# Optimization experiments

Hardware: AMD Instinct MI355X
Metric: run time of the kernel (lower is better)

The kernel has to match this reference:

```python
import jax, jax.numpy as jnp
import numpy as np

# Static trigram-LM trie configuration (uniform branching K per node).
V_ = 32000; N_ = 3; K_ = 32; S_ = 32; SOS_ = 0; B_ = 32; L_ = 8
U_ = V_ + 1
N_BI = V_ * K_                    # number of bigram nodes
O_ = U_ + N_BI + 1                # offsets/logbs length (bigram block + sentinel)
N_TRI = N_BI * K_                 # number of trigram leaves
G_ = N_TRI
P_ = O_ + G_                      # logps length


def _build_trie():
    """Valid CSR-style flattened trie: children of node at position q live at
    [offsets[q]+q, offsets[q+1]+q+1); every node has exactly K children with
    sorted token ids 0..K-1. ids[p-U_] is the token id of node at position p."""
    rng = np.random.default_rng(0)
    offsets = np.empty(O_, np.int64)
    # unigram v's children occupy positions [U_+v*K_, U_+(v+1)*K_)
    offsets[:U_] = U_ + np.arange(U_) * (K_ - 1)
    # bigram j (position U_+j) children occupy [O_+j*K_, O_+(j+1)*K_)
    offsets[U_:] = (O_ - U_) + np.arange(N_BI + 1) * (K_ - 1)
    ids = np.empty(P_ - U_, np.int32)
    ids[:N_BI] = np.arange(N_BI) % K_       # bigram node token ids
    ids[N_BI] = 0                           # sentinel slot at position O_-1
    ids[N_BI + 1:] = np.arange(N_TRI) % K_  # trigram leaf token ids
    logps = (-rng.uniform(0.1, 10.0, P_)).astype(np.float32)
    logbs = (-rng.uniform(0.01, 2.0, O_)).astype(np.float32)
    return offsets.astype(np.int32), ids, logps, logbs


def setup_inputs() -> dict:
    key = jax.random.key(0)
    k1, k2 = jax.random.split(key)
    offsets, ids, logps, logbs = _build_trie()
    # tokens in [0, 2K): half of them miss in the trie -> exercises backoff path
    hist = jax.random.randint(k1, (L_, B_), 0, 2 * K_, dtype=jnp.int32)
    hidx = jax.random.randint(k2, (B_,), 0, L_, dtype=jnp.int32)
    return {"hist": hist, "hidx": hidx, "offsets": jnp.asarray(offsets),
            "ids": jnp.asarray(ids), "logps": jnp.asarray(logps),
            "logbs": jnp.asarray(logbs), "sos": SOS_, "V": V_, "N": N_,
            "G": G_, "S": S_}


def reference(hist, hidx, offsets, ids, logps, logbs, sos, V, N, G, S):
    B = hist.shape[1]
    M = B * V
    O = offsets.shape[0]
    P = logps.shape[0]
    shift = 0 if 0 <= sos < V else 1
    U = V + shift + 1 % N
    if N == 1:
        return jnp.broadcast_to(logps[:V], (B, V))
    # Always left-pad N-1 sos tokens (equivalent to torch's rem padding; the
    # subsequent window gather makes extra padding harmless).
    pad = N - 1
    hist = jnp.concatenate([jnp.full((pad, B), sos, hist.dtype), hist])
    hidx = hidx + pad
    # context = the N-1 tokens at positions hidx-(N-1) .. hidx-1, per batch
    pos = hidx[None, :] - (N - 1) + jnp.arange(N - 1)[:, None]   # (N-1, B)
    ctx = jnp.take_along_axis(hist, pos, axis=0)                  # (N-1, B)
    if shift:
        ctx = jnp.where(ctx == sos, V, ctx)
    ctx = ctx.astype(ids.dtype)
    srange = jnp.arange(S)
    # first M entries: candidate words v per batch; last B: context pointer
    desc = jnp.concatenate([jnp.tile(jnp.arange(V, dtype=jnp.int32), B),
                            ctx[-1].astype(jnp.int32)])
    last_logps = jnp.tile(logps[:V], B)                           # (M,)
    last_backoffs = jnp.repeat(logbs[desc[M:]], V)                # (M,)
    found = jnp.ones(M + B, bool)
    for n in range(1, N):
        hist_n = jnp.concatenate([jnp.repeat(ctx[-n], V), ctx[-min(n + 1, N - 1)]])
        desc_starts = offsets[desc] + desc
        desc_ends = offsets[desc + 1] + desc + 1
        pos_desc = desc_starts[:, None] + srange[None, :]         # (M+B, S)
        ext = desc_ends[:, None] > pos_desc
        ids_ = ids[jnp.minimum(pos_desc, P - 1) - U]
        ext = ext & (hist_n[:, None] == ids_)
        found = ext.any(1) & found
        desc = jnp.where(found, jnp.where(ext, pos_desc, 0).sum(1), desc)
        logps_desc = logps[desc[:M]]
        if n == N - 1:
            cur_backoffs = jnp.zeros_like(last_backoffs)
        else:
            cur_backoffs = jnp.repeat(
                jnp.where(found[M:], logbs[jnp.minimum(desc[M:], O - 1)], 0.0), V)
        clobber = jnp.isfinite(logps_desc) & found[:M]
        cur_logps = jnp.where(clobber, logps_desc,
                              last_logps + cur_backoffs + last_backoffs)
        last_backoffs = jnp.where(clobber, cur_backoffs, 0.0)
        last_logps = jnp.where(jnp.repeat(hidx >= n, V), cur_logps, last_logps)
    return last_logps.reshape(B, V)
```

## Files before the change

### kernel.cpp

```cpp
#include <hip/hip_runtime.h>
#include <math.h>


#define MAXN 8
#define TPB  1024
#define NW   16
#define BGW  2
#define BGB  32
#define WI   37
#define WO   41

struct PerB {
  int   ctx[MAXN];
  float bo[MAXN];
  float b1;
  int   hp;
};

__device__ __forceinline__ bool find_child(const int* __restrict__ offsets,
                                           const int* __restrict__ ids,
                                           int q, int t, int U, int P, int S,
                                           int* pos_out) {
  int start = offsets[q] + q;
  int end   = offsets[q + 1] + q + 1;
  int n = end - start;
  if (n > S) n = S;
  if (n <= 0) return false;
  int j = (t < n - 1) ? t : (n - 1);
  if (j < 0) j = 0;
  int x = ids[min(start + j, P - 1) - U];
  if (x == t) { *pos_out = start + j; return true; }
  if (x < t) return false;
  int lo = 0, hi = j - 1;
  while (lo < hi) {
    int mid = (lo + hi) >> 1;
    int xm = ids[min(start + mid, P - 1) - U];
    if (xm < t) lo = mid + 1; else hi = mid;
  }
  if (lo < j) {
    int xm = ids[min(start + lo, P - 1) - U];
    if (xm == t) { *pos_out = start + lo; return true; }
  }
  return false;
}

__device__ __forceinline__ float score_v(const int* __restrict__ offsets,
                                         const int* __restrict__ ids,
                                         const float* __restrict__ logps,
                                         const PerB* __restrict__ pbb,
                                         int v, float lp0,
                                         int N, int U, int O, int P, int S) {
  float last_lp = lp0;
  float last_bo = pbb->b1;
  int hp = pbb->hp;
  int desc = v;
  bool found = true;
  float cur_lp = lp0;
  for (int n = 1; n <= N - 1; ++n) {
    int t = pbb->ctx[(N - 1) - n];
    if (found) {
      int pos;
      found = find_child(offsets, ids, desc, t, U, P, S, &pos);
      if (found) { desc = pos; cur_lp = logps[desc]; }
    }
    float cur_bo = (n == N - 1) ? 0.0f : pbb->bo[n];
    bool clobber = isfinite(cur_lp) && found;
    float newlp = clobber ? cur_lp : (last_lp + cur_bo + last_bo);
    last_bo = clobber ? cur_bo : 0.0f;
    if (hp >= n) last_lp = newlp;
  }
  return last_lp;
}

__global__ void __launch_bounds__(TPB, 8)
lm_fused(const int* __restrict__ hist, const int* __restrict__ hidx,
         const int* __restrict__ offsets, const int* __restrict__ ids,
         const float* __restrict__ logps, const float* __restrict__ logbs,
         const int* __restrict__ sos_p, const int* __restrict__ N_p,
         const int* __restrict__ S_p,
         float* __restrict__ out,
         int V, int B, int L, int O, int P) {
  __shared__ PerB s_pb[BGB];
  __shared__ int  ids_w[64 * WI];
  __shared__ int  off_w[64 * WO];
  __shared__ int  s_start1[64], s_n1[64], s_shi[64], s_sho[64];

  const int tid  = threadIdx.x;
  const int lane = tid & 63;
  const int w    = tid >> 6;
  const int vbase = blockIdx.x * 64;
  const int v     = vbase + lane;
  const int b0    = blockIdx.y * BGB;
  const int N = *N_p, S = *S_p, sos = *sos_p;
  const int Nc = (N > 0) ? N : 1;
  const int shift = (0 <= sos && sos < V) ? 0 : 1;
  const int U = V + shift + 1 % Nc;
  const int idsN = P - U;

  const bool fast = (N == 3) && (S == 32);

  if (tid < BGB && N > 1) {
    int b = b0 + tid;
    if (b < B) {
      int pad = N - 1;
      int hp = hidx[b] + pad;
      PerB o;
      o.hp = hp;
      for (int k = 0; k < N - 1; ++k) {
        int r = hp - (N - 1) + k;
        int tok = (r < pad) ? sos : hist[(r - pad) * B + b];
        if (shift && tok == sos) tok = V;
        o.ctx[k] = tok;
      }
      o.b1 = logbs[o.ctx[N - 2]];
      int desc = o.ctx[N - 2];
      bool found = true;
      for (int n = 1; n <= N - 2; ++n) {
        int t = o.ctx[(N - 1) - min(n + 1, N - 1)];
        if (found) {
          int pos;
          found = find_child(offsets, ids, desc, t, U, P, S, &pos);
          if (found) desc = pos;
        }
        o.bo[n] = found ? logbs[min(desc, O - 1)] : 0.0f;
      }
      s_pb[tid] = o;
    }
  }

  if (!fast) {
    __syncthreads();
    if (v < V) {
      float lp0 = logps[v];
      if (N <= 1) {
        for (int ib = w; ib < BGB; ib += NW) {
          int b = b0 + ib;
          if (b < B) out[(size_t)b * V + v] = lp0;
        }
      } else {
        for (int ib = w; ib < BGB; ib += NW) {
          int b = b0 + ib;
          if (b < B)
            out[(size_t)b * V + v] = score_v(offsets, ids, logps, s_pb + ib, v,
                                             lp0, N, U, O, P, S);
        }
      }
    }
    return;
  }

  {
    int row  = tid >> 4;
    int part = tid & 15;
    int vv = vbase + row;
    if (vv < V) {
      int ov  = offsets[vv];
      int ov1 = offsets[vv + 1];
      int start1 = ov + vv;
      int n1 = ov1 + 1 - ov;
      if (n1 > 32) n1 = 32;
      int* myids = ids_w + row * WI;
      int* myoff = off_w + row * WO;
      int aidx0 = start1 - U;
      int sh_i = 0, sh_o = 0;
      bool vec_ok = (start1 >= 0) && (aidx0 >= 0) &&
                    (((aidx0 & ~3) + 36) <= idsN) &&
                    (((start1 & ~3) + 40) <= O);
      if (vec_ok) {
        int ab = aidx0 & ~3;
        sh_i = aidx0 - ab;
        const int4* ip = (const int4*)(ids + ab);
        for (int k = part; k < 9; k += 16) {
          int4 t = ip[k];
          myids[4 * k + 0] = t.x; myids[4 * k + 1] = t.y;
          myids[4 * k + 2] = t.z; myids[4 * k + 3] = t.w;
        }
        int ob = start1 & ~3;
        sh_o = start1 - ob;
        const int4* op = (const int4*)(offsets + ob);
        for (int k = part; k < 10; k += 16) {
          int4 t = op[k];
          myoff[4 * k + 0] = t.x; myoff[4 * k + 1] = t.y;
          myoff[4 * k + 2] = t.z; myoff[4 * k + 3] = t.w;
        }
      } else {
        for (int j = part; j < 36; j += 16) {
          int ii = min(start1 + j, P - 1) - U;
          ii = max(0, min(ii, idsN - 1));
          myids[j] = ids[ii];
        }
        for (int j = part; j < 40; j += 16) {
          int oo = max(0, min(start1 + j, O - 1));
          myoff[j] = offsets[oo];
        }
      }
      if (part == 0) {
        s_start1[row] = start1; s_n1[row] = n1;
        s_shi[row] = sh_i;      s_sho[row] = sh_o;
      }
    } else if (part == 0) {
      s_start1[row] = 0; s_n1[row] = 0; s_shi[row] = 0; s_sho[row] = 0;
    }
  }
  __syncthreads();
  if (v >= V) return;

  float lp0 = logps[v];
  const int start1 = s_start1[lane];
  const int n1     = s_n1[lane];
  const int sh_i   = s_shi[lane];
  const int sh_o   = s_sho[lane];
  const int* myids = ids_w + lane * WI;
  const int* myoff = off_w + lane * WO;

  const int nb = min(BGB, B - b0);

  int j1v[BGW];
  int cc1[BGW];
  int cc2[BGW];
  unsigned f1m = 0, l2m = 0;
#pragma unroll
  for (int i = 0; i < BGW; ++i) {
    int ib = w * BGW + i;
    if (ib >= nb) { j1v[i] = 0; cc1[i] = v; cc2[i] = v; continue; }
    int t1 = s_pb[ib].ctx[1];
    bool found = false;
    int j1 = 0;
    if (n1 > 0) {
      int jj = (t1 < n1 - 1) ? t1 : (n1 - 1);
      if (jj < 0) jj = 0;
      int x = myids[sh_i + jj];
      if (x == t1) { found = true; j1 = jj; }
      else if (x > t1) {
        int lo = 0, hi = jj - 1;
        while (lo < hi) {
          int mid = (lo + hi) >> 1;
          if (myids[sh_i + mid] < t1) lo = mid + 1; else hi = mid;
        }
        if (lo < jj && myids[sh_i + lo] == t1) { found = true; j1 = lo; }
      }
    }
    int c1 = start1 + j1;
    j1v[i] = j1;
    int a1 = min(c1, P - 1);
    cc1[i] = a1;
    int t0 = s_pb[ib].ctx[0];
    int o1 = myoff[sh_o + j1];
    int o2 = myoff[sh_o + j1 + 1];
    int start2 = o1 + c1;
    int n2 = o2 + 1 - o1;
    if (n2 > 32) n2 = 32;
    bool l2ok = found && (n2 > 0);
    int jj2 = (t0 < n2 - 1) ? t0 : (n2 - 1);
    if (jj2 < 0) jj2 = 0;
    int c2 = min(start2 + jj2, P - 1);
    cc2[i] = l2ok ? c2 : a1;
    f1m |= (found ? 1u : 0u) << i;
    l2m |= (l2ok ? 1u : 0u) << i;
  }

  float lp1v[BGW];
  int   x2v[BGW];
#pragma unroll
  for (int i = 0; i < BGW; ++i) lp1v[i] = logps[cc1[i]];
#pragma unroll
  for (int i = 0; i < BGW; ++i) {
    int ii = cc2[i] - U;
    ii = max(0, min(ii, idsN - 1));
    x2v[i] = __builtin_nontemporal_load(ids + ii);
  }

  float sp2v[BGW];
#pragma unroll
  for (int i = 0; i < BGW; ++i) {
    int ib = w * BGW + i;
    sp2v[i] = 0.0f;
    if (ib < nb) {
      bool l2ok = (l2m >> i) & 1u;
      if (l2ok && x2v[i] == s_pb[ib].ctx[0])
        sp2v[i] = __builtin_nontemporal_load(logps + cc2[i]);
    }
  }

#pragma unroll
  for (int i = 0; i < BGW; ++i) {
    int ib = w * BGW + i;
    if (ib >= nb) continue;
    bool found = (f1m >> i) & 1u;
    bool l2ok  = (l2m >> i) & 1u;
    int   hp = s_pb[ib].hp;
    float bo1 = s_pb[ib].bo[1];
    float last_bo = s_pb[ib].b1;
    float last_lp = lp0;

    float lp1 = found ? lp1v[i] : lp0;
    bool clob = found && isfinite(lp1);
    float nl = clob ? lp1 : (last_lp + bo1 + last_bo);
    last_bo = clob ? bo1 : 0.0f;
    if (hp >= 1) last_lp = nl;

    bool f2 = false;
    float lp2 = 0.0f;
    if (l2ok) {
      int t0 = s_pb[ib].ctx[0];
      int x2 = x2v[i];
      if (x2 == t0) { f2 = true; lp2 = sp2v[i]; }
      else if (x2 > t0) {
        int j1 = j1v[i];
        int c1 = start1 + j1;
        int o1 = myoff[sh_o + j1];
        int o2 = myoff[sh_o + j1 + 1];
        int start2 = o1 + c1;
        int n2 = o2 + 1 - o1;
        if (n2 > 32) n2 = 32;
        int jj2 = (t0 < n2 - 1) ? t0 : (n2 - 1);
        if (jj2 < 0) jj2 = 0;
        int lo = 0, hi = jj2 - 1;
        while (lo < hi) {
          int mid = (lo + hi) >> 1;
          int im = max(0, min(min(start2 + mid, P - 1) - U, idsN - 1));
          if (ids[im] < t0) lo = mid + 1; else hi = mid;
        }
        if (lo < jj2) {
          int il = max(0, min(min(start2 + lo, P - 1) - U, idsN - 1));
          if (ids[il] == t0) { f2 = true; lp2 = logps[min(start2 + lo, P - 1)]; }
        }
      }
    }
    bool clob2 = f2 && isfinite(lp2);
    float nl2 = clob2 ? lp2 : (last_lp + last_bo);
    if (hp >= 2) last_lp = nl2;

    __builtin_nontemporal_store(last_lp, out + (size_t)(b0 + ib) * V + v);
  }
}

extern "C" void kernel_launch(void* const* d_in, const int* in_sizes, int n_in,
                              void* d_out, int out_size, void* d_ws, size_t ws_size,
                              hipStream_t stream) {
  const int*   hist    = (const int*)d_in[0];
  const int*   hidx    = (const int*)d_in[1];
  const int*   offsets = (const int*)d_in[2];
  const int*   ids     = (const int*)d_in[3];
  const float* logps   = (const float*)d_in[4];
  const float* logbs   = (const float*)d_in[5];
  const int*   sos_p   = (const int*)d_in[6];
  const int*   N_p     = (const int*)d_in[8];
  const int*   S_p     = (const int*)d_in[10];

  int B = in_sizes[1];
  int L = in_sizes[0] / B;
  int O = in_sizes[2];
  int P = in_sizes[4];
  int V = out_size / B;
  float* out = (float*)d_out;

  dim3 grid((V + 63) / 64, (B + BGB - 1) / BGB);
  lm_fused<<<grid, dim3(TPB), 0, stream>>>(
      hist, hidx, offsets, ids, logps, logbs, sos_p, N_p, S_p, out,
      V, B, L, O, P);
}
```

Baseline: 264.4 us.

## Remap threads so each 16-lane group handles one vocab entry with sorted batches

Changes the work mapping so that 16 consecutive threads share one vocabulary node and each processes two batch rows, with batch rows ordered by their context token so neighbouring lanes probe nearby trie entries. Results are staged in a shared-memory tile and then written out coalesced per batch row after an extra barrier. The goal is better locality of the gathered ids/logps loads within a wavefront. The cost is the rank computation, more shared memory and an additional synchronisation.

After: 259.8 us. About the same (-1.8%).

```diff
diff --git a/kernel.cpp b/kernel.cpp
--- a/kernel.cpp
+++ b/kernel.cpp
@@ -80,22 +80,24 @@
          const int* __restrict__ S_p,
          float* __restrict__ out,
          int V, int B, int L, int O, int P) {
-  __shared__ PerB s_pb[BGB];
-  __shared__ int  ids_w[64 * WI];
-  __shared__ int  off_w[64 * WO];
-  __shared__ int  s_start1[64], s_n1[64], s_shi[64], s_sho[64];
+  __shared__ PerB  s_pb[BGB];
+  __shared__ int   ids_w[64 * WI];
+  __shared__ int   off_w[64 * WO];
+  __shared__ int   s_start1[64], s_n1[64], s_shi[64], s_sho[64];
+  __shared__ int   s_order[BGB];
+  __shared__ float s_res[BGB][65];
 
   const int tid  = threadIdx.x;
   const int lane = tid & 63;
   const int w    = tid >> 6;
   const int vbase = blockIdx.x * 64;
-  const int v     = vbase + lane;
   const int b0    = blockIdx.y * BGB;
   const int N = *N_p, S = *S_p, sos = *sos_p;
   const int Nc = (N > 0) ? N : 1;
   const int shift = (0 <= sos && sos < V) ? 0 : 1;
   const int U = V + shift + 1 % Nc;
   const int idsN = P - U;
+  const int nb = min(BGB, B - b0);
 
   const bool fast = (N == 3) && (S == 32);
 
@@ -125,11 +127,21 @@
         o.bo[n] = found ? logbs[min(desc, O - 1)] : 0.0f;
       }
       s_pb[tid] = o;
+      if (fast) {
+        int myt1 = o.ctx[1];
+        int r = 0;
+        for (int b2 = 0; b2 < nb; ++b2) {
+          int t1b = s_pb[b2].ctx[1];
+          r += (t1b < myt1) || (t1b == myt1 && b2 < tid);
+        }
+        s_order[r] = tid;
+      }
     }
   }
 
   if (!fast) {
     __syncthreads();
+    int v = vbase + lane;
     if (v < V) {
       float lp0 = logps[v];
       if (N <= 1) {
@@ -203,27 +215,36 @@
     }
   }
   __syncthreads();
-  if (v >= V) return;
-
-  float lp0 = logps[v];
-  const int start1 = s_start1[lane];
-  const int n1     = s_n1[lane];
-  const int sh_i   = s_shi[lane];
-  const int sh_o   = s_sho[lane];
-  const int* myids = ids_w + lane * WI;
-  const int* myoff = off_w + lane * WO;
-
-  const int nb = min(BGB, B - b0);
-
+
+  const int g  = tid >> 4;
+  const int sl = tid & 15;
+  const int v  = vbase + g;
+  const bool vok = (v < V);
+
+  float lp0 = vok ? logps[v] : 0.0f;
+  const int start1 = s_start1[g];
+  const int n1     = s_n1[g];
+  const int sh_i   = s_shi[g];
+  const int sh_o   = s_sho[g];
+  const int* myids = ids_w + g * WI;
+  const int* myoff = off_w + g * WO;
+
+  int bidx[BGW];
   int j1v[BGW];
   int cc1[BGW];
   int cc2[BGW];
   unsigned f1m = 0, l2m = 0;
 #pragma unroll
   for (int i = 0; i < BGW; ++i) {
-    int ib = w * BGW + i;
-    if (ib >= nb) { j1v[i] = 0; cc1[i] = v; cc2[i] = v; continue; }
-    int t1 = s_pb[ib].ctx[1];
+    int k = sl * BGW + i;
+    if (!vok || k >= nb) {
+      bidx[i] = -1; j1v[i] = 0;
+      cc1[i] = vok ? v : 0; cc2[i] = cc1[i];
+      continue;
+    }
+    int b = s_order[k];
+    bidx[i] = b;
+    int t1 = s_pb[b].ctx[1];
     bool found = false;
     int j1 = 0;
     if (n1 > 0) {
@@ -244,7 +265,7 @@
     j1v[i] = j1;
     int a1 = min(c1, P - 1);
     cc1[i] = a1;
-    int t0 = s_pb[ib].ctx[0];
+    int t0 = s_pb[b].ctx[0];
     int o1 = myoff[sh_o + j1];
     int o2 = myoff[sh_o + j1 + 1];
     int start2 = o1 + c1;
@@ -273,24 +294,23 @@
   float sp2v[BGW];
 #pragma unroll
   for (int i = 0; i < BGW; ++i) {
-    int ib = w * BGW + i;
     sp2v[i] = 0.0f;
-    if (ib < nb) {
+    if (bidx[i] >= 0) {
       bool l2ok = (l2m >> i) & 1u;
-      if (l2ok && x2v[i] == s_pb[ib].ctx[0])
+      if (l2ok && x2v[i] == s_pb[bidx[i]].ctx[0])
         sp2v[i] = __builtin_nontemporal_load(logps + cc2[i]);
     }
   }
 
 #pragma unroll
   for (int i = 0; i < BGW; ++i) {
-    int ib = w * BGW + i;
-    if (ib >= nb) continue;
+    int b = bidx[i];
+    if (b < 0) continue;
     bool found = (f1m >> i) & 1u;
     bool l2ok  = (l2m >> i) & 1u;
-    int   hp = s_pb[ib].hp;
-    float bo1 = s_pb[ib].bo[1];
-    float last_bo = s_pb[ib].b1;
+    int   hp = s_pb[b].hp;
+    float bo1 = s_pb[b].bo[1];
+    float last_bo = s_pb[b].b1;
     float last_lp = lp0;
 
     float lp1 = found ? lp1v[i] : lp0;
@@ -302,7 +322,7 @@
     bool f2 = false;
     float lp2 = 0.0f;
     if (l2ok) {
-      int t0 = s_pb[ib].ctx[0];
+      int t0 = s_pb[b].ctx[0];
       int x2 = x2v[i];
       if (x2 == t0) { f2 = true; lp2 = sp2v[i]; }
       else if (x2 > t0) {
@@ -331,7 +351,17 @@
     float nl2 = clob2 ? lp2 : (last_lp + last_bo);
     if (hp >= 2) last_lp = nl2;
 
-    __builtin_nontemporal_store(last_lp, out + (size_t)(b0 + ib) * V + v);
+    s_res[b][g] = last_lp;
+  }
+
+  __syncthreads();
+#pragma unroll
+  for (int q = 0; q < 2; ++q) {
+    int ib = w * 2 + q;
+    int vv = vbase + lane;
+    if (ib < nb && vv < V)
+      __builtin_nontemporal_store(s_res[ib][lane],
+                                  out + (size_t)(b0 + ib) * V + vv);
   }
 }
 
```
